# Kernel optimization log

Measured on AMD Instinct MI355X. Metric: run time of the kernel, lower is better.

## Reference

```python
import jax, jax.numpy as jnp
import numpy as np

EMBED_DIM = 1024
N_HEADS = 16
HEAD_DIM = EMBED_DIM // N_HEADS


def setup_inputs() -> dict:
    key = jax.random.key(0)
    k1, k2, k3 = jax.random.split(key, 3)
    B, T, D = 2, 2048, EMBED_DIM
    x = jax.random.normal(k1, (B, T, D), dtype=jnp.float32)
    # torch nn.Linear weights: (out_features, in_features); y = x @ W.T
    scale = 1.0 / np.sqrt(D)
    qkv_w = jax.random.uniform(k2, (3 * D, D), dtype=jnp.float32, minval=-scale, maxval=scale)
    out_w = jax.random.uniform(k3, (D, D), dtype=jnp.float32, minval=-scale, maxval=scale)
    return {"x": x, "qkv_w": qkv_w, "out_w": out_w}


def reference(x, qkv_w, out_w):
    B, T, D = x.shape
    H, hd = N_HEADS, HEAD_DIM
    qkv = jnp.einsum('btd,ed->bte', x, qkv_w)  # (B,T,3D)
    qkv = qkv.reshape(B, T, 3, H, hd)
    q = jnp.transpose(qkv[:, :, 0], (0, 2, 1, 3))  # (B,H,T,hd)
    k = jnp.transpose(qkv[:, :, 1], (0, 2, 1, 3))
    v = jnp.transpose(qkv[:, :, 2], (0, 2, 1, 3))
    scores = jnp.einsum('bhtd,bhsd->bhts', q, k) / np.sqrt(hd).astype(np.float32)
    causal = jnp.tril(jnp.ones((T, T), dtype=bool))  # True = keep
    scores = jnp.where(causal[None, None], scores, -jnp.inf)
    probs = jax.nn.softmax(scores, axis=-1)
    out = jnp.einsum('bhts,bhsd->bhtd', probs, v)
    out = jnp.transpose(out, (0, 2, 1, 3)).reshape(B, T, D)
    return jnp.einsum('btd,ed->bte', out, out_w)
```

## Files before the change

### kernel.cpp

```cpp
#include <hip/hip_runtime.h>
#include <hip/hip_bf16.h>
#include <stdint.h>

typedef __bf16 bf16;
typedef __attribute__((ext_vector_type(8))) __bf16 bf16x8;
typedef __attribute__((ext_vector_type(4))) __bf16 bf16x4;
typedef __attribute__((ext_vector_type(4))) float f32x4;

#define AS1 __attribute__((address_space(1)))
#define AS3 __attribute__((address_space(3)))

__device__ __forceinline__ void async16(const void* g, void* l) {
  __builtin_amdgcn_global_load_lds((AS1 uint32_t*)(g), (AS3 uint32_t*)(l), 16, 0, 0);
}

__device__ __forceinline__ f32x4 mfma_bf16(bf16x8 a, bf16x8 b, f32x4 c) {
  return __builtin_amdgcn_mfma_f32_16x16x32_bf16(a, b, c, 0, 0, 0);
}

__device__ __forceinline__ uint32_t pack2_bf16(float a, float b) {
  union { __hip_bfloat162 h2; uint32_t u; } u;
  u.h2 = __float22bfloat162_rn(float2{a, b});
  return u.u;
}

__global__ __launch_bounds__(256) void cast_all_kernel(
    const float* __restrict__ x, const float* __restrict__ w1,
    const float* __restrict__ w2, bf16* __restrict__ xb,
    bf16* __restrict__ w1b, bf16* __restrict__ w2b) {
  const int bid = blockIdx.x;
  const float* src;
  bf16* dst;
  int base;
  if (bid < 4096) { src = x;  dst = xb;  base = bid; }
  else if (bid < 7168) { src = w1; dst = w1b; base = bid - 4096; }
  else { src = w2; dst = w2b; base = bid - 7168; }
  const int i = (base * 256 + threadIdx.x) * 4;
  const float4 v = *(const float4*)(src + i);
  bf16x4 o;
  o[0] = (bf16)v.x; o[1] = (bf16)v.y; o[2] = (bf16)v.z; o[3] = (bf16)v.w;
  *(bf16x4*)(dst + i) = o;
}

__global__ __launch_bounds__(256) void gemm_qkv_kernel(
    const bf16* __restrict__ A, const bf16* __restrict__ W,
    bf16* __restrict__ QK, bf16* __restrict__ VT) {
  constexpr int K = 1024;
  __shared__ __align__(16) bf16 sm[2 * 128 * 32];
  const int tid = threadIdx.x;
  const int w = tid >> 6, lane = tid & 63;
  const int m0 = blockIdx.x * 128, n0 = blockIdx.y * 128;
  const int wm = (w >> 1) * 64, wn = (w & 1) * 64;
  const int lrow = lane & 15, quad = lane >> 4;
  const int lk = quad * 8;
  f32x4 acc[4][4] = {};

  for (int k0 = 0; k0 < K; k0 += 32) {
#pragma unroll
    for (int i = 0; i < 4; ++i) {
      const int c = tid + 256 * i;
      const bf16* src = (c < 512)
          ? (A + (size_t)(m0 + (c >> 2)) * K + k0 + (c & 3) * 8)
          : (W + (size_t)(n0 + ((c - 512) >> 2)) * K + k0 + (c & 3) * 8);
      async16(src, sm + (w * 64 + i * 256) * 8);
    }
    __syncthreads();
    bf16x8 af[4], bfr[4];
#pragma unroll
    for (int mi = 0; mi < 4; ++mi)
      af[mi] = *(const bf16x8*)&sm[(wm + mi * 16 + lrow) * 32 + lk];
#pragma unroll
    for (int ni = 0; ni < 4; ++ni)
      bfr[ni] = *(const bf16x8*)&sm[128 * 32 + (wn + ni * 16 + lrow) * 32 + lk];
#pragma unroll
    for (int mi = 0; mi < 4; ++mi)
#pragma unroll
      for (int ni = 0; ni < 4; ++ni)
        acc[mi][ni] = mfma_bf16(af[mi], bfr[ni], acc[mi][ni]);
    __syncthreads();
  }

  bf16* s2 = sm;
  const bool isV = (n0 >= 2048);
  const int bb = m0 >> 11;
  const int mt = m0 & 2047;
  if (!isV) {
#pragma unroll
    for (int c = 0; c < 2; ++c) {
      if ((w >> 1) == c) {
#pragma unroll
        for (int mi = 0; mi < 4; ++mi)
#pragma unroll
          for (int ni = 0; ni < 4; ++ni) {
            const int nr = wn + ni * 16 + lrow;
#pragma unroll
            for (int r = 0; r < 4; ++r)
              s2[(mi * 16 + quad * 4 + r) * 128 + nr] = (bf16)acc[mi][ni][r];
          }
      }
      __syncthreads();
#pragma unroll
      for (int p = 0; p < 4; ++p) {
        const int row = p * 16 + (tid >> 4);
        const int colc = (tid & 15) * 8;
        const bf16x8 v = *(const bf16x8*)&s2[row * 128 + colc];
        *(bf16x8*)(QK + (size_t)(m0 + c * 64 + row) * 2048 + n0 + colc) = v;
      }
      __syncthreads();
    }
  } else {
#pragma unroll
    for (int c = 0; c < 2; ++c) {
      if ((w & 1) == c) {
#pragma unroll
        for (int mi = 0; mi < 4; ++mi)
#pragma unroll
          for (int ni = 0; ni < 4; ++ni) {
            const int nl = ni * 16 + lrow;
            bf16x4 pk4;
#pragma unroll
            for (int r = 0; r < 4; ++r) pk4[r] = (bf16)acc[mi][ni][r];
            *(bf16x4*)&s2[nl * 128 + wm + mi * 16 + quad * 4] = pk4;
          }
      }
      __syncthreads();
#pragma unroll
      for (int p = 0; p < 4; ++p) {
        const int row = p * 16 + (tid >> 4);
        const int colc = (tid & 15) * 8;
        const bf16x8 v = *(const bf16x8*)&s2[row * 128 + colc];
        const int vtrow = bb * 1024 + (n0 - 2048) + c * 64 + row;
        *(bf16x8*)(VT + (size_t)vtrow * 2048 + mt + colc) = v;
      }
      __syncthreads();
    }
  }
}

__global__ __launch_bounds__(256) void attn_kernel(
    const bf16* __restrict__ QK, const bf16* __restrict__ VT,
    bf16* __restrict__ AO) {
  __shared__ __align__(16) bf16 sK[2][2][64 * 64];
  __shared__ __align__(16) bf16 sV[2][2][64 * 64];
  const int bid = blockIdx.x;
  const int bh = bid & 31;
  const int bp = (bid >> 5) & 7;
  const int sub = bid >> 8;
  const int b = bh >> 4, hd = bh & 15;
  const int tid = threadIdx.x, w = tid >> 6, lane = tid & 63;
  const int col = lane & 15, quad = lane >> 4;
  const bf16* Qb = QK + (size_t)b * 2048 * 2048 + hd * 64;
  const bf16* Kb = Qb + 1024;
  const bf16* Vb = VT + (size_t)bh * 64 * 2048;
  const float NEG_INF = -__builtin_inff();
  constexpr float QSCALE = 0.18033688011112042f;
  const int n0 = 16 - bp;

  union { uint32_t u[4]; bf16x8 v; } ones;
  ones.u[0] = 0x3F803F80u; ones.u[1] = 0x3F803F80u;
  ones.u[2] = 0x3F803F80u; ones.u[3] = 0x3F803F80u;

  const int RA = (15 - bp) * 128 + sub * 64 + w * 16;
  const int RB = bp * 128 + sub * 64 + w * 16;
  const int qrowA = RA + col, qrowB = RB + col;
  bf16x8 qfA[2], qfB[2];
#pragma unroll
  for (int kk = 0; kk < 2; ++kk) {
    bf16x8 v0 = *(const bf16x8*)(Qb + (size_t)qrowA * 2048 + kk * 32 + quad * 8);
    bf16x8 v1 = *(const bf16x8*)(Qb + (size_t)qrowB * 2048 + kk * 32 + quad * 8);
#pragma unroll
    for (int e = 0; e < 8; ++e) {
      v0[e] = (bf16)((float)v0[e] * QSCALE);
      v1[e] = (bf16)((float)v1[e] * QSCALE);
    }
    qfA[kk] = v0; qfB[kk] = v1;
  }

  auto stage = [&](int s0, int c) {
    bf16* dK = &sK[c][0][0];
    bf16* dV = &sV[c][0][0];
#pragma unroll
    for (int i2 = 0; i2 < 4; ++i2) {
      const int L = tid + 256 * i2;
      const int buf = L >> 9, Lr = L & 511;
      const int row = Lr >> 3;
      const int ch = (Lr & 7) ^ (row & 7);
      async16(Kb + (size_t)(s0 + buf * 64 + row) * 2048 + ch * 8, dK + L * 8);
    }
#pragma unroll
    for (int i2 = 0; i2 < 4; ++i2) {
      const int L = tid + 256 * i2;
      const int buf = L >> 9, Lr = L & 511;
      const int d = Lr >> 3;
      const int ch = (Lr & 7) ^ (d & 7);
      async16(Vb + (size_t)d * 2048 + s0 + buf * 64 + ch * 8, dV + L * 8);
    }
  };

  int srow[4];
#pragma unroll
  for (int m = 0; m < 4; ++m)
    srow[m] = 32 * (m & 1) + (col >> 2) * 8 + 4 * (m >> 1) + (col & 3);

  f32x4 accO[4] = {};
  f32x4 accL = {};

  auto body = [&](const bf16* kbuf, const bf16* vbuf, const bf16x8* qf,
                  int kv0, int qrowv, bool masked) {
    f32x4 st[4] = {};
#pragma unroll
    for (int kk = 0; kk < 2; ++kk) {
      bf16x8 kf[4];
#pragma unroll
      for (int m = 0; m < 4; ++m)
        kf[m] = *(const bf16x8*)&kbuf[srow[m] * 64 + (((kk * 4 + quad) ^ (srow[m] & 7)) * 8)];
      __builtin_amdgcn_s_setprio(1);
#pragma unroll
      for (int m = 0; m < 4; ++m)
        st[m] = mfma_bf16(kf[m], qf[kk], st[m]);
      __builtin_amdgcn_s_setprio(0);
    }

    if (masked) {
#pragma unroll
      for (int m = 0; m < 4; ++m) {
        const int kvb = kv0 + 32 * (m & 1) + quad * 8 + 4 * (m >> 1);
#pragma unroll
        for (int r = 0; r < 4; ++r)
          st[m][r] = (kvb + r <= qrowv) ? st[m][r] : NEG_INF;
      }
    }

    uint32_t pk[4][2];
#pragma unroll
    for (int m = 0; m < 4; ++m) {
      const float p0 = __builtin_amdgcn_exp2f(st[m][0]);
      const float p1 = __builtin_amdgcn_exp2f(st[m][1]);
      const float p2 = __builtin_amdgcn_exp2f(st[m][2]);
      const float p3 = __builtin_amdgcn_exp2f(st[m][3]);
      pk[m][0] = pack2_bf16(p0, p1);
      pk[m][1] = pack2_bf16(p2, p3);
    }

#pragma unroll
    for (int kk = 0; kk < 2; ++kk) {
      bf16x8 vf[4];
#pragma unroll
      for (int d = 0; d < 4; ++d) {
        const int row = d * 16 + col;
        vf[d] = *(const bf16x8*)&vbuf[row * 64 + (((kk * 4 + quad) ^ (row & 7)) * 8)];
      }
      union { uint32_t u[4]; bf16x8 v; } f;
      f.u[0] = pk[kk][0];
      f.u[1] = pk[kk][1];
      f.u[2] = pk[2 + kk][0];
      f.u[3] = pk[2 + kk][1];
      __builtin_amdgcn_s_setprio(1);
      accL = mfma_bf16(ones.v, f.v, accL);
#pragma unroll
      for (int d = 0; d < 4; ++d)
        accO[d] = mfma_bf16(vf[d], f.v, accO[d]);
      __builtin_amdgcn_s_setprio(0);
    }
  };

  auto writeout = [&](int qrowv) {
    bf16* Ob = AO + (size_t)b * 2048 * 1024 + hd * 64;
    const float inv = 1.0f / accL[0];
#pragma unroll
    for (int d = 0; d < 4; ++d) {
      bf16x4 o;
#pragma unroll
      for (int r = 0; r < 4; ++r) o[r] = (bf16)(accO[d][r] * inv);
      *(bf16x4*)(Ob + (size_t)qrowv * 1024 + d * 16 + quad * 4) = o;
    }
  };

  stage(0, 0);
  int cur = 0;
  for (int i = 0; i < 17; ++i) {
    if (i + 1 < 17) {
      const int nx = (i + 1 < n0) ? (i + 1) : (i + 1 - n0);
      stage(nx * 128, cur ^ 1);
      asm volatile("s_waitcnt vmcnt(8)" ::: "memory");
    } else {
      asm volatile("s_waitcnt vmcnt(0)" ::: "memory");
    }
    __builtin_amdgcn_s_barrier();
    const bool inH = (i < n0);
    const int j = inH ? i : i - n0;
    const int Rw = inH ? RA : RB;
    const int qrowv = inH ? qrowA : qrowB;
    const bf16x8* qf = inH ? qfA : qfB;
    const int kv0 = j * 128;
    if (kv0 <= Rw + 15)
      body(&sK[cur][0][0], &sV[cur][0][0], qf, kv0, qrowv, kv0 + 63 > Rw);
    if (kv0 + 64 <= Rw + 15)
      body(&sK[cur][1][0], &sV[cur][1][0], qf, kv0 + 64, qrowv, kv0 + 127 > Rw);
    if (i == n0 - 1) {
      writeout(qrowA);
#pragma unroll
      for (int d = 0; d < 4; ++d) accO[d] = f32x4{0.f, 0.f, 0.f, 0.f};
      accL = f32x4{0.f, 0.f, 0.f, 0.f};
    }
    __builtin_amdgcn_s_barrier();
    cur ^= 1;
  }
  writeout(qrowB);
}

__global__ __launch_bounds__(256) void gemm_out_kernel(
    const bf16* __restrict__ A, const bf16* __restrict__ W,
    float* __restrict__ C) {
  constexpr int K = 1024;
  __shared__ __align__(16) bf16 sm[2 * 128 * 32];
  const int tid = threadIdx.x;
  const int w = tid >> 6, lane = tid & 63;
  const int m0 = blockIdx.x * 128, n0 = blockIdx.y * 128;
  const int wm = (w >> 1) * 64, wn = (w & 1) * 64;
  const int lrow = lane & 15, lk = (lane >> 4) * 8;
  f32x4 acc[4][4] = {};

  for (int k0 = 0; k0 < K; k0 += 32) {
#pragma unroll
    for (int i = 0; i < 4; ++i) {
      const int c = tid + 256 * i;
      const bf16* src = (c < 512)
          ? (A + (size_t)(m0 + (c >> 2)) * K + k0 + (c & 3) * 8)
          : (W + (size_t)(n0 + ((c - 512) >> 2)) * K + k0 + (c & 3) * 8);
      async16(src, sm + (w * 64 + i * 256) * 8);
    }
    __syncthreads();
    bf16x8 af[4], bfr[4];
#pragma unroll
    for (int mi = 0; mi < 4; ++mi)
      af[mi] = *(const bf16x8*)&sm[(wm + mi * 16 + lrow) * 32 + lk];
#pragma unroll
    for (int ni = 0; ni < 4; ++ni)
      bfr[ni] = *(const bf16x8*)&sm[128 * 32 + (wn + ni * 16 + lrow) * 32 + lk];
#pragma unroll
    for (int mi = 0; mi < 4; ++mi)
#pragma unroll
      for (int ni = 0; ni < 4; ++ni)
        acc[mi][ni] = mfma_bf16(af[mi], bfr[ni], acc[mi][ni]);
    __syncthreads();
  }

#pragma unroll
  for (int mi = 0; mi < 4; ++mi)
#pragma unroll
    for (int ni = 0; ni < 4; ++ni) {
      const int n = n0 + wn + ni * 16 + lrow;
#pragma unroll
      for (int r = 0; r < 4; ++r) {
        const int m = m0 + wm + mi * 16 + (lane >> 4) * 4 + r;
        C[(size_t)m * 1024 + n] = acc[mi][ni][r];
      }
    }
}

extern "C" void kernel_launch(void* const* d_in, const int* in_sizes, int n_in,
                              void* d_out, int out_size, void* d_ws, size_t ws_size,
                              hipStream_t stream) {
  const float* x     = (const float*)d_in[0];
  const float* qkv_w = (const float*)d_in[1];
  const float* out_w = (const float*)d_in[2];
  float* out = (float*)d_out;

  char* ws = (char*)d_ws;
  bf16* xb    = (bf16*)(ws);
  bf16* aob   = (bf16*)(ws);
  bf16* wqkvb = (bf16*)(ws + 8u * 1024 * 1024);
  bf16* wob   = (bf16*)(ws + 14u * 1024 * 1024);
  bf16* qkb   = (bf16*)(ws + 16u * 1024 * 1024);
  bf16* vtb   = (bf16*)(ws + 32u * 1024 * 1024);

  cast_all_kernel<<<8192, 256, 0, stream>>>(x, qkv_w, out_w, xb, wqkvb, wob);
  gemm_qkv_kernel<<<dim3(32, 24), 256, 0, stream>>>(xb, wqkvb, qkb, vtb);
  attn_kernel<<<dim3(512), 256, 0, stream>>>(qkb, vtb, aob);
  gemm_out_kernel<<<dim3(32, 8), 256, 0, stream>>>(aob, wob, out);
}
```

Before: 170.2 us.

## Split attention into 128-thread blocks with 32-row query tiles and 64-wide KV stages

Attention now launches 1024 blocks of two waves instead of 512 blocks of four. Each block covers 32 query rows per band and stages one 64-key K/V tile at a time instead of two. Per-block tile counts now follow the causal extent of its rows, so fewer fully masked tiles are loaded. The aim is more blocks for load balance and occupancy, at the cost of each staged K/V tile being shared by fewer waves, more barriers per key, and more total global-to-LDS traffic.

```diff
diff --git a/kernel.cpp b/kernel.cpp
--- a/kernel.cpp
+++ b/kernel.cpp
@@ -137,15 +137,15 @@
   }
 }
 
-__global__ __launch_bounds__(256) void attn_kernel(
+__global__ __launch_bounds__(128) void attn_kernel(
     const bf16* __restrict__ QK, const bf16* __restrict__ VT,
     bf16* __restrict__ AO) {
-  __shared__ __align__(16) bf16 sK[2][2][64 * 64];
-  __shared__ __align__(16) bf16 sV[2][2][64 * 64];
+  __shared__ __align__(16) bf16 sK[2][64 * 64];
+  __shared__ __align__(16) bf16 sV[2][64 * 64];
   const int bid = blockIdx.x;
   const int bh = bid & 31;
   const int bp = (bid >> 5) & 7;
-  const int sub = bid >> 8;
+  const int s = bid >> 8;
   const int b = bh >> 4, hd = bh & 15;
   const int tid = threadIdx.x, w = tid >> 6, lane = tid & 63;
   const int col = lane & 15, quad = lane >> 4;
@@ -154,14 +154,17 @@
   const bf16* Vb = VT + (size_t)bh * 64 * 2048;
   const float NEG_INF = -__builtin_inff();
   constexpr float QSCALE = 0.18033688011112042f;
-  const int n0 = 16 - bp;
+  const int bandH = 15 - bp, bandL = bp;
+  const int sH = s, sL = 3 - s;
+  const int nH = 2 * bandH + 1 + (sH >> 1);
+  const int nL = 2 * bandL + 1 + (sL >> 1);
 
   union { uint32_t u[4]; bf16x8 v; } ones;
   ones.u[0] = 0x3F803F80u; ones.u[1] = 0x3F803F80u;
   ones.u[2] = 0x3F803F80u; ones.u[3] = 0x3F803F80u;
 
-  const int RA = (15 - bp) * 128 + sub * 64 + w * 16;
-  const int RB = bp * 128 + sub * 64 + w * 16;
+  const int RA = bandH * 128 + sH * 32 + w * 16;
+  const int RB = bandL * 128 + sL * 32 + w * 16;
   const int qrowA = RA + col, qrowB = RB + col;
   bf16x8 qfA[2], qfB[2];
 #pragma unroll
@@ -177,23 +180,21 @@
   }
 
   auto stage = [&](int s0, int c) {
-    bf16* dK = &sK[c][0][0];
-    bf16* dV = &sV[c][0][0];
+    bf16* dK = &sK[c][0];
+    bf16* dV = &sV[c][0];
 #pragma unroll
     for (int i2 = 0; i2 < 4; ++i2) {
-      const int L = tid + 256 * i2;
-      const int buf = L >> 9, Lr = L & 511;
-      const int row = Lr >> 3;
-      const int ch = (Lr & 7) ^ (row & 7);
-      async16(Kb + (size_t)(s0 + buf * 64 + row) * 2048 + ch * 8, dK + L * 8);
+      const int L = tid + 128 * i2;
+      const int row = L >> 3;
+      const int ch = (L & 7) ^ (row & 7);
+      async16(Kb + (size_t)(s0 + row) * 2048 + ch * 8, dK + L * 8);
     }
 #pragma unroll
     for (int i2 = 0; i2 < 4; ++i2) {
-      const int L = tid + 256 * i2;
-      const int buf = L >> 9, Lr = L & 511;
-      const int d = Lr >> 3;
-      const int ch = (Lr & 7) ^ (d & 7);
-      async16(Vb + (size_t)d * 2048 + s0 + buf * 64 + ch * 8, dV + L * 8);
+      const int L = tid + 128 * i2;
+      const int d = L >> 3;
+      const int ch = (L & 7) ^ (d & 7);
+      async16(Vb + (size_t)d * 2048 + s0 + ch * 8, dV + L * 8);
     }
   };
 
@@ -276,28 +277,26 @@
     }
   };
 
+  const int nT = nH + nL;
   stage(0, 0);
   int cur = 0;
-  for (int i = 0; i < 17; ++i) {
-    if (i + 1 < 17) {
-      const int nx = (i + 1 < n0) ? (i + 1) : (i + 1 - n0);
-      stage(nx * 128, cur ^ 1);
+  for (int i = 0; i < nT; ++i) {
+    if (i + 1 < nT) {
+      const int nx = (i + 1 < nH) ? (i + 1) : (i + 1 - nH);
+      stage(nx * 64, cur ^ 1);
       asm volatile("s_waitcnt vmcnt(8)" ::: "memory");
     } else {
       asm volatile("s_waitcnt vmcnt(0)" ::: "memory");
     }
     __builtin_amdgcn_s_barrier();
-    const bool inH = (i < n0);
-    const int j = inH ? i : i - n0;
+    const bool inH = (i < nH);
+    const int kv0 = (inH ? i : i - nH) * 64;
     const int Rw = inH ? RA : RB;
     const int qrowv = inH ? qrowA : qrowB;
     const bf16x8* qf = inH ? qfA : qfB;
-    const int kv0 = j * 128;
     if (kv0 <= Rw + 15)
-      body(&sK[cur][0][0], &sV[cur][0][0], qf, kv0, qrowv, kv0 + 63 > Rw);
-    if (kv0 + 64 <= Rw + 15)
-      body(&sK[cur][1][0], &sV[cur][1][0], qf, kv0 + 64, qrowv, kv0 + 127 > Rw);
-    if (i == n0 - 1) {
+      body(&sK[cur][0], &sV[cur][0], qf, kv0, qrowv, kv0 + 63 > Rw);
+    if (i == nH - 1) {
       writeout(qrowA);
 #pragma unroll
       for (int d = 0; d < 4; ++d) accO[d] = f32x4{0.f, 0.f, 0.f, 0.f};
@@ -377,6 +376,6 @@
 
   cast_all_kernel<<<8192, 256, 0, stream>>>(x, qkv_w, out_w, xb, wqkvb, wob);
   gemm_qkv_kernel<<<dim3(32, 24), 256, 0, stream>>>(xb, wqkvb, qkb, vtb);
-  attn_kernel<<<dim3(512), 256, 0, stream>>>(qkb, vtb, aob);
+  attn_kernel<<<dim3(1024), 128, 0, stream>>>(qkb, vtb, aob);
   gemm_out_kernel<<<dim3(32, 8), 256, 0, stream>>>(aob, wob, out);
 }
```

Measured after the change: 186.3 us. 1.09x slower.
